# Optimization experiments

Hardware: AMD Instinct MI355X
Metric: run time of the kernel (lower is better)

Reference implementation:

```python
import jax, jax.numpy as jnp
import numpy as np

B, TQ, TKV, D, H = 4, 1024, 2048, 1024, 16
DH = D // H


def setup_inputs() -> dict:
    key = jax.random.key(0)
    ks = jax.random.split(key, 12)
    s = 0.02
    return {
        "x": jax.random.normal(ks[0], (B, TQ, D), jnp.float32),
        "k_cache": jax.random.normal(ks[1], (B, TKV, D), jnp.float32),
        "v_cache": jax.random.normal(ks[2], (B, TKV, D), jnp.float32),
        "mask": jnp.zeros((TQ, TKV), jnp.float32),  # additive attention bias
        "Wq": jax.random.normal(ks[3], (D, D), jnp.float32) * s,
        "bq": jax.random.normal(ks[4], (D,), jnp.float32) * s,
        "Wk": jax.random.normal(ks[5], (D, D), jnp.float32) * s,  # key: no bias (Whisper-style)
        "Wv": jax.random.normal(ks[6], (D, D), jnp.float32) * s,
        "bv": jax.random.normal(ks[7], (D,), jnp.float32) * s,
        "Wo": jax.random.normal(ks[8], (D, D), jnp.float32) * s,
        "bo": jax.random.normal(ks[9], (D,), jnp.float32) * s,
    }


def reference(x, k_cache, v_cache, mask, Wq, bq, Wk, Wv, bv, Wo, bo):
    b, tq, d = x.shape
    scale = (d // H) ** -0.25
    # QKV projections (torch Linear: y = x @ W.T + b)
    q = x @ Wq.T + bq                      # [B,Tq,D]
    k_new = x @ Wk.T                       # [B,Tq,D] (key has no bias)
    v_new = x @ Wv.T + bv                  # [B,Tq,D]
    # KV-cache append: write last Tq positions
    k_cache = k_cache.at[:, -tq:, :].set(k_new)
    v_cache = v_cache.at[:, -tq:, :].set(v_new)
    # split heads
    qh = q.reshape(b, tq, H, DH) * scale           # [B,Tq,H,Dh]
    kh = k_cache.reshape(b, -1, H, DH) * scale     # [B,Tkv,H,Dh]
    vh = v_cache.reshape(b, -1, H, DH)             # [B,Tkv,H,Dh]
    qk = jnp.einsum("bqhd,bkhd->bhqk", qh, kh) + mask  # [B,H,Tq,Tkv]
    w = jax.nn.softmax(qk.astype(jnp.float32), axis=-1).astype(qh.dtype)
    wv = jnp.einsum("bhqk,bkhd->bqhd", w, vh).reshape(b, tq, d)
    out = wv @ Wo.T + bo
    return out, k_cache, v_cache
```

## Files before the change

### kernel.cpp

```cpp
#include <hip/hip_runtime.h>
#include <hip/hip_bf16.h>


typedef __bf16 bf16_t;
typedef __attribute__((ext_vector_type(4))) float f32x4;
typedef __attribute__((ext_vector_type(4))) float f4v;
typedef __attribute__((ext_vector_type(8))) __bf16 bf16x8;
typedef __attribute__((ext_vector_type(4))) __bf16 bf16x4;
typedef __attribute__((ext_vector_type(4))) unsigned short u16x4;

__device__ inline bf16x4 cvt4v(f4v f) {
    bf16x4 o;
    o.x = (bf16_t)f.x; o.y = (bf16_t)f.y; o.z = (bf16_t)f.z; o.w = (bf16_t)f.w;
    return o;
}

__device__ inline void gload_lds16(const void* g, void* s) {
    __builtin_amdgcn_global_load_lds(
        (const __attribute__((address_space(1))) void*)g,
        (__attribute__((address_space(3))) void*)s, 16, 0, 0);
}

__device__ inline bf16x8 ldsr128(const bf16_t* p) {
    bf16x8 d;
    unsigned a = (unsigned)(size_t)(const __attribute__((address_space(3))) bf16_t*)p;
    asm volatile("ds_read_b128 %0, %1" : "=v"(d) : "v"(a));
    return d;
}

#define WAIT_LGKM0 do { asm volatile("s_waitcnt lgkmcnt(0)" ::: "memory"); \
                        __builtin_amdgcn_sched_barrier(0); } while (0)
#define WAIT_VM(n) asm volatile("s_waitcnt vmcnt(" #n ")" ::: "memory")

__device__ inline unsigned cvt_pk_bf16(float lo, float hi) {
    unsigned r;
    asm("v_cvt_pk_bf16_f32 %0, %1, %2" : "=v"(r) : "v"(lo), "v"(hi));
    return r;
}
__device__ inline void pswap32(unsigned& a, unsigned& b) {
    asm("v_permlane32_swap_b32 %0, %1" : "+v"(a), "+v"(b));
}
__device__ inline void pswap16(unsigned& a, unsigned& b) {
    asm("v_permlane16_swap_b32 %0, %1" : "+v"(a), "+v"(b));
}

#if __has_builtin(__builtin_amdgcn_exp2f)
__device__ inline float exp2_fast(float x) { return __builtin_amdgcn_exp2f(x); }
#else
__device__ inline float exp2_fast(float x) { return exp2f(x); }
#endif

__global__ __launch_bounds__(256) void prep_all_k(
        const float* __restrict__ x, const float* __restrict__ kc,
        const float* __restrict__ vc, const float* __restrict__ mask,
        const float* __restrict__ Wq, const float* __restrict__ Wk,
        const float* __restrict__ Wv, const float* __restrict__ Wo,
        const float* __restrict__ bq, const float* __restrict__ bv,
        bf16_t* __restrict__ x_bf, bf16_t* __restrict__ wqkv_bf,
        bf16_t* __restrict__ wo_bf, float* __restrict__ bias,
        bf16_t* __restrict__ maskB, float* __restrict__ kout,
        float* __restrict__ vout, bf16_t* __restrict__ k_bf,
        bf16_t* __restrict__ vT) {
    __shared__ bf16_t tsh[64][65];
    int blk = blockIdx.x, tid = threadIdx.x;
    if (blk < 1024) {
        int kvt = blk >> 6;
        int bh  = blk & 63;
        int b = bh >> 4, h = bh & 15;
        int kv0 = kvt * 64;
        int c = tid & 63, r0 = tid >> 6;
        #pragma unroll
        for (int rr = r0; rr < 64; rr += 4)
            tsh[rr][c] = (bf16_t)vc[((size_t)b * 2048 + kv0 + rr) * 1024 + h * 64 + c];
        __syncthreads();
        #pragma unroll
        for (int dd = r0; dd < 64; dd += 4)
            vT[((size_t)bh * 64 + dd) * 2048 + kv0 + c] = tsh[c][dd];
    } else if (blk < 9216) {
        int i = (blk - 1024) * 256 + tid;
        int which = i >> 20;
        int ii = i & 1048575;
        int b = ii >> 18;
        int r = ii & 262143;
        size_t off = (size_t)b * 2097152 + (size_t)r * 4;
        if (which == 0) {
            f4v f = __builtin_nontemporal_load(reinterpret_cast<const f4v*>(kc + off));
            __builtin_nontemporal_store(f, reinterpret_cast<f4v*>(kout + off));
            __builtin_nontemporal_store(cvt4v(f), reinterpret_cast<bf16x4*>(k_bf + off));
        } else {
            f4v f = *reinterpret_cast<const f4v*>(vc + off);
            __builtin_nontemporal_store(f, reinterpret_cast<f4v*>(vout + off));
        }
    } else if (blk < 13312) {
        int i = (blk - 9216) * 256 + tid;
        f4v f = __builtin_nontemporal_load(reinterpret_cast<const f4v*>(x) + i);
        reinterpret_cast<bf16x4*>(x_bf)[i] = cvt4v(f);
    } else if (blk < 16384) {
        int i = (blk - 13312) * 256 + tid;
        int e0 = i * 4;
        int row = e0 >> 10;
        const float* src;
        if (row < 1024)       src = Wq + e0;
        else if (row < 2048)  src = Wk + (e0 - 1048576);
        else                  src = Wv + (e0 - 2097152);
        f4v f = __builtin_nontemporal_load(reinterpret_cast<const f4v*>(src));
        reinterpret_cast<bf16x4*>(wqkv_bf)[i] = cvt4v(f);
    } else if (blk < 24576) {
        int i = (blk - 16384) * 256 + tid;
        int r   = i & 3;
        int c16 = (i >> 2) & 15;
        int qd  = (i >> 6) & 3;
        int kb  = (i >> 8) & 127;
        int qb  = i >> 15;
        float v = mask[(size_t)(qb * 16 + c16) * 2048 + kb * 16 + qd * 4 + r] * 1.4426950408889634f;
        maskB[i] = (bf16_t)v;
    } else if (blk < 25600) {
        int i = (blk - 24576) * 256 + tid;
        f4v f = __builtin_nontemporal_load(reinterpret_cast<const f4v*>(Wo) + i);
        reinterpret_cast<bf16x4*>(wo_bf)[i] = cvt4v(f);
    } else {
        int i = (blk - 25600) * 256 + tid;
        if (i < 3072) {
            float v;
            if (i < 1024)      v = bq[i];
            else if (i < 2048) v = 0.f;
            else               v = bv[i - 2048];
            bias[i] = v;
        }
    }
}

__global__ __launch_bounds__(256) void transpose_v_k(const float* __restrict__ vout,
                                                     bf16_t* __restrict__ vT) {
    __shared__ bf16_t t[64][65];
    int blk = blockIdx.x;
    int kvt = blk >> 6;
    int bh  = blk & 63;
    int b = bh >> 4, h = bh & 15;
    int kv0 = 1024 + kvt * 64;
    int tid = threadIdx.x;
    int c = tid & 63, r0 = tid >> 6;
    #pragma unroll
    for (int rr = r0; rr < 64; rr += 4)
        t[rr][c] = (bf16_t)vout[((size_t)b * 2048 + kv0 + rr) * 1024 + h * 64 + c];
    __syncthreads();
    #pragma unroll
    for (int dd = r0; dd < 64; dd += 4)
        vT[((size_t)bh * 64 + dd) * 2048 + kv0 + c] = t[c][dd];
}

__global__ __launch_bounds__(512, 2) void gemm8_k(const bf16_t* __restrict__ A,
                                                  const bf16_t* __restrict__ Bw,
                                                  const float* __restrict__ bias,
                                                  bf16_t* __restrict__ q_bf,
                                                  float* __restrict__ kout,
                                                  bf16_t* __restrict__ k_bf,
                                                  float* __restrict__ vout) {
    const int K = 1024;
    __shared__ __align__(16) bf16_t As[2][16384];
    __shared__ __align__(16) bf16_t Bs[2][16384];
    int flat = blockIdx.y * 16 + blockIdx.x;
    int logi = (flat & 7) * 24 + (flat >> 3);
    int m0 = (logi / 12) * 256, n0 = (logi % 12) * 256;
    int tid = threadIdx.x;
    int lane = tid & 63, w = tid >> 6;
    int wrM = w >> 2, wrN = w & 3;
    int col16 = lane & 15, quad = lane >> 4;
    int cx = (quad ^ (col16 & 7)) * 8;

    int sr = tid >> 3;
    int scb = ((tid & 7) ^ (sr & 7)) * 8;
    const bf16_t* ga = A + (size_t)(m0 + sr) * K + scb;
    const bf16_t* gb = Bw + (size_t)(n0 + sr) * K + scb;
    int ldst = sr * 64 + (tid & 7) * 8;

    auto stageA = [&](int d, int kt) {
        size_t ko = (size_t)kt * 64;
        gload_lds16(ga + ko, &As[d][ldst]);
        gload_lds16(ga + 64 * (size_t)K + ko, &As[d][ldst + 4096]);
        gload_lds16(ga + 128 * (size_t)K + ko, &As[d][ldst + 8192]);
        gload_lds16(ga + 192 * (size_t)K + ko, &As[d][ldst + 12288]);
    };
    auto stageB = [&](int d, int kt) {
        size_t ko = (size_t)kt * 64;
        gload_lds16(gb + ko, &Bs[d][ldst]);
        gload_lds16(gb + 64 * (size_t)K + ko, &Bs[d][ldst + 4096]);
        gload_lds16(gb + 128 * (size_t)K + ko, &Bs[d][ldst + 8192]);
        gload_lds16(gb + 192 * (size_t)K + ko, &Bs[d][ldst + 12288]);
    };

    int arow = wrM * 128 + col16;
    int brow = wrN * 64 + col16;

    f32x4 zero = {0.f, 0.f, 0.f, 0.f};
    f32x4 acc[8][4];
    #pragma unroll
    for (int mi = 0; mi < 8; mi++)
        #pragma unroll
        for (int ni = 0; ni < 4; ni++) acc[mi][ni] = zero;

    stageA(0, 0);
    stageB(0, 0);
    stageA(1, 1);
    WAIT_VM(4);
    __builtin_amdgcn_s_barrier();

    for (int kt = 0; kt < 16; kt++) {
        int d = kt & 1;
        const bf16_t* Ad = As[d];
        const bf16_t* Bd = Bs[d];
        bf16x8 a0[4][2], bb0[2][2];
        #pragma unroll
        for (int mi = 0; mi < 4; mi++) {
            const bf16_t* p = &Ad[(arow + mi * 16) * 64];
            a0[mi][0] = ldsr128(p + cx);
            a0[mi][1] = ldsr128(p + (cx ^ 32));
        }
        #pragma unroll
        for (int ni = 0; ni < 2; ni++) {
            const bf16_t* p = &Bd[(brow + ni * 16) * 64];
            bb0[ni][0] = ldsr128(p + cx);
            bb0[ni][1] = ldsr128(p + (cx ^ 32));
        }
        if (kt < 15) stageB(d ^ 1, kt + 1);
        __builtin_amdgcn_s_barrier();
        WAIT_LGKM0;
        __builtin_amdgcn_s_setprio(1);
        #pragma unroll
        for (int mi = 0; mi < 4; mi++)
            #pragma unroll
            for (int ni = 0; ni < 2; ni++) {
                acc[mi][ni] = __builtin_amdgcn_mfma_f32_16x16x32_bf16(a0[mi][0], bb0[ni][0], acc[mi][ni], 0, 0, 0);
                acc[mi][ni] = __builtin_amdgcn_mfma_f32_16x16x32_bf16(a0[mi][1], bb0[ni][1], acc[mi][ni], 0, 0, 0);
            }
        __builtin_amdgcn_s_setprio(0);
        __builtin_amdgcn_s_barrier();
        bf16x8 bb1[2][2];
        #pragma unroll
        for (int ni = 0; ni < 2; ni++) {
            const bf16_t* p = &Bd[(brow + 32 + ni * 16) * 64];
            bb1[ni][0] = ldsr128(p + cx);
            bb1[ni][1] = ldsr128(p + (cx ^ 32));
        }
        __builtin_amdgcn_s_barrier();
        WAIT_LGKM0;
        __builtin_amdgcn_s_setprio(1);
        #pragma unroll
        for (int mi = 0; mi < 4; mi++)
            #pragma unroll
            for (int ni = 0; ni < 2; ni++) {
                acc[mi][ni + 2] = __builtin_amdgcn_mfma_f32_16x16x32_bf16(a0[mi][0], bb1[ni][0], acc[mi][ni + 2], 0, 0, 0);
                acc[mi][ni + 2] = __builtin_amdgcn_mfma_f32_16x16x32_bf16(a0[mi][1], bb1[ni][1], acc[mi][ni + 2], 0, 0, 0);
            }
        __builtin_amdgcn_s_setprio(0);
        __builtin_amdgcn_s_barrier();
        bf16x8 a1[4][2];
        #pragma unroll
        for (int mi = 0; mi < 4; mi++) {
            const bf16_t* p = &Ad[(arow + 64 + mi * 16) * 64];
            a1[mi][0] = ldsr128(p + cx);
            a1[mi][1] = ldsr128(p + (cx ^ 32));
        }
        __builtin_amdgcn_s_barrier();
        WAIT_LGKM0;
        __builtin_amdgcn_s_setprio(1);
        #pragma unroll
        for (int mi = 0; mi < 4; mi++)
            #pragma unroll
            for (int ni = 0; ni < 2; ni++) {
                acc[mi + 4][ni] = __builtin_amdgcn_mfma_f32_16x16x32_bf16(a1[mi][0], bb0[ni][0], acc[mi + 4][ni], 0, 0, 0);
                acc[mi + 4][ni] = __builtin_amdgcn_mfma_f32_16x16x32_bf16(a1[mi][1], bb0[ni][1], acc[mi + 4][ni], 0, 0, 0);
            }
        __builtin_amdgcn_s_setprio(0);
        __builtin_amdgcn_s_barrier();
        if (kt < 14) {
            stageA(d, kt + 2);
            WAIT_VM(4);
        } else {
            WAIT_VM(0);
        }
        __builtin_amdgcn_s_barrier();
        __builtin_amdgcn_s_setprio(1);
        #pragma unroll
        for (int mi = 0; mi < 4; mi++)
            #pragma unroll
            for (int ni = 0; ni < 2; ni++) {
                acc[mi + 4][ni + 2] = __builtin_amdgcn_mfma_f32_16x16x32_bf16(a1[mi][0], bb1[ni][0], acc[mi + 4][ni + 2], 0, 0, 0);
                acc[mi + 4][ni + 2] = __builtin_amdgcn_mfma_f32_16x16x32_bf16(a1[mi][1], bb1[ni][1], acc[mi + 4][ni + 2], 0, 0, 0);
            }
        __builtin_amdgcn_s_setprio(0);
        __builtin_amdgcn_s_barrier();
    }

    int mb = m0 + wrM * 128 + quad * 4;
    int nb = n0 + wrN * 64 + col16;
    if (n0 < 1024) {
        #pragma unroll
        for (int ni = 0; ni < 4; ni++) {
            int gn = nb + ni * 16;
            float bia = bias[gn];
            #pragma unroll
            for (int mi = 0; mi < 8; mi++) {
                int gm = mb + mi * 16;
                #pragma unroll
                for (int r = 0; r < 4; r++)
                    __builtin_nontemporal_store((bf16_t)(acc[mi][ni][r] + bia),
                                                &q_bf[(size_t)(gm + r) * 1024 + gn]);
            }
        }
    } else if (n0 < 2048) {
        #pragma unroll
        for (int ni = 0; ni < 4; ni++) {
            int gn = nb + ni * 16;
            float bia = bias[gn];
            int n2 = gn - 1024;
            #pragma unroll
            for (int mi = 0; mi < 8; mi++) {
                int gm = mb + mi * 16;
                #pragma unroll
                for (int r = 0; r < 4; r++) {
                    int gmr = gm + r;
                    int b = gmr >> 10, t = gmr & 1023;
                    size_t off = ((size_t)b * 2048 + 1024 + t) * 1024 + n2;
                    float v = acc[mi][ni][r] + bia;
                    __builtin_nontemporal_store(v, &kout[off]);
                    __builtin_nontemporal_store((bf16_t)v, &k_bf[off]);
                }
            }
        }
    } else {
        #pragma unroll
        for (int ni = 0; ni < 4; ni++) {
            int gn = nb + ni * 16;
            float bia = bias[gn];
            int n2 = gn - 2048;
            #pragma unroll
            for (int mi = 0; mi < 8; mi++) {
                int gm = mb + mi * 16;
                #pragma unroll
                for (int r = 0; r < 4; r++) {
                    int gmr = gm + r;
                    int b = gmr >> 10, t = gmr & 1023;
                    __builtin_nontemporal_store(acc[mi][ni][r] + bia,
                        &vout[((size_t)b * 2048 + 1024 + t) * 1024 + n2]);
                }
            }
        }
    }
}

__global__ __launch_bounds__(256) void gemm_wo_k(const bf16_t* __restrict__ A,
                                                 const bf16_t* __restrict__ Bw,
                                                 const float* __restrict__ bias,
                                                 float* __restrict__ out0) {
    const int K = 1024;
    __shared__ __align__(16) bf16_t As[2][4096];
    __shared__ __align__(16) bf16_t Bs[2][4096];
    int m0 = blockIdx.x * 128, n0 = blockIdx.y * 128;
    int tid = threadIdx.x;
    int lane = tid & 63, w = tid >> 6;
    int wr = w >> 1, wc = w & 1;
    int col16 = lane & 15, quad = lane >> 4;

    int srow = tid >> 2;
    int scol = ((tid & 3) ^ ((srow >> 1) & 3)) * 8;
    const bf16_t* ga = A + (size_t)(m0 + srow) * K + scol;
    const bf16_t* gb = Bw + (size_t)(n0 + srow) * K + scol;

    int qsw = (quad ^ ((col16 >> 1) & 3)) * 8;

    f32x4 zero = {0.f, 0.f, 0.f, 0.f};
    f32x4 acc[4][4];
    #pragma unroll
    for (int mi = 0; mi < 4; mi++)
        #pragma unroll
        for (int ni = 0; ni < 4; ni++) acc[mi][ni] = zero;

    auto stageg = [&](int d, int k) {
        gload_lds16(ga + k, &As[d][tid * 8]);
        gload_lds16(ga + (size_t)64 * K + k, &As[d][tid * 8 + 2048]);
        gload_lds16(gb + k, &Bs[d][tid * 8]);
        gload_lds16(gb + (size_t)64 * K + k, &Bs[d][tid * 8 + 2048]);
    };

    stageg(0, 0);
    __syncthreads();
    for (int kb = 0; kb < 32; kb++) {
        int cur = kb & 1;
        if (kb < 31) stageg(cur ^ 1, (kb + 1) * 32);
        bf16x8 af[4], bfr[4];
        #pragma unroll
        for (int mi = 0; mi < 4; mi++)
            af[mi] = ldsr128(&As[cur][(wr * 64 + mi * 16 + col16) * 32 + qsw]);
        #pragma unroll
        for (int ni = 0; ni < 4; ni++)
            bfr[ni] = ldsr128(&Bs[cur][(wc * 64 + ni * 16 + col16) * 32 + qsw]);
        WAIT_LGKM0;
        #pragma unroll
        for (int mi = 0; mi < 4; mi++)
            #pragma unroll
            for (int ni = 0; ni < 4; ni++)
                acc[mi][ni] = __builtin_amdgcn_mfma_f32_16x16x32_bf16(
                    af[mi], bfr[ni], acc[mi][ni], 0, 0, 0);
        __syncthreads();
    }

    int mbase = m0 + wr * 64 + quad * 4;
    int nbase = n0 + wc * 64 + col16;
    #pragma unroll
    for (int ni = 0; ni < 4; ni++) {
        int gn = nbase + ni * 16;
        float bia = bias[gn];
        #pragma unroll
        for (int mi = 0; mi < 4; mi++) {
            int gm = mbase + mi * 16;
            #pragma unroll
            for (int r = 0; r < 4; r++)
                __builtin_nontemporal_store(acc[mi][ni][r] + bia,
                                            &out0[(size_t)(gm + r) * 1024 + gn]);
        }
    }
}

__global__ __launch_bounds__(512, 4) void attn_k(const bf16_t* __restrict__ qbf,
                                                 const bf16_t* __restrict__ kbf,
                                                 const bf16_t* __restrict__ vT,
                                                 const bf16_t* __restrict__ maskB,
                                                 bf16_t* __restrict__ wv) {
    __shared__ __align__(16) bf16_t Ks[2][4096];
    __shared__ __align__(16) bf16_t Vs[2][4096];
    int logical = (blockIdx.x & 7) * 64 + (blockIdx.x >> 3);
    int bh = logical >> 3;
    int qtb = logical & 7;
    int b = bh >> 4, h = bh & 15;
    int tid = threadIdx.x, w = tid >> 6, lane = tid & 63;
    int col16 = lane & 15, quad = lane >> 4;
    int c7 = col16 & 7;
    int cx = (quad ^ c7) * 8;
    int qr0 = qtb * 128 + w * 16;

    int sr = tid >> 3, sc = (tid & 7) ^ ((tid >> 3) & 7);
    const bf16_t* kg = kbf + ((size_t)b * 2048 + sr) * 1024 + h * 64 + sc * 8;
    const bf16_t* vg = vT + ((size_t)bh * 64 + sr) * 2048 + sc * 8;
    auto stage = [&](int d, int kv0) {
        gload_lds16(kg + (size_t)kv0 * 1024, &Ks[d][tid * 8]);
        gload_lds16(vg + kv0, &Vs[d][tid * 8]);
    };

    const bf16_t* qrow = qbf + ((size_t)b * 1024 + qr0 + col16) * 1024 + h * 64;
    bf16x8 aq0 = *reinterpret_cast<const bf16x8*>(qrow + quad * 8);
    bf16x8 aq1 = *reinterpret_cast<const bf16x8*>(qrow + 32 + quad * 8);

    const bf16_t* mbase = maskB + (size_t)(qtb * 8 + w) * 32768 + quad * 64 + col16 * 4;

    f32x4 zero = {0.f, 0.f, 0.f, 0.f};
    f32x4 oacc[4];
    #pragma unroll
    for (int dt = 0; dt < 4; dt++) oacc[dt] = zero;
    float lrow = 0.f;

    stage(0, 0);
    __syncthreads();

    for (int t = 0; t < 32; t++) {
        int cur = t & 1;
        if (t < 31) stage(cur ^ 1, (t + 1) * 64);
        bf16x8 kf[4][2];
        #pragma unroll
        for (int nt = 0; nt < 4; nt++) {
            const bf16_t* kr = &Ks[cur][(nt * 16 + col16) * 64];
            kf[nt][0] = ldsr128(kr + cx);
            kf[nt][1] = ldsr128(kr + (cx ^ 32));
        }
        u16x4 m4[4];
        #pragma unroll
        for (int nt = 0; nt < 4; nt++)
            m4[nt] = *reinterpret_cast<const u16x4*>(mbase + (size_t)(t * 4 + nt) * 256);
        WAIT_LGKM0;
        f32x4 sv[4];
        __builtin_amdgcn_s_setprio(1);
        #pragma unroll
        for (int nt = 0; nt < 4; nt++) {
            sv[nt] = __builtin_amdgcn_mfma_f32_16x16x32_bf16(kf[nt][0], aq0, zero, 0, 0, 0);
            sv[nt] = __builtin_amdgcn_mfma_f32_16x16x32_bf16(kf[nt][1], aq1, sv[nt], 0, 0, 0);
        }
        __builtin_amdgcn_s_setprio(0);
        unsigned pk[4][2];
        #pragma unroll
        for (int nt = 0; nt < 4; nt++) {
            float p[4];
            #pragma unroll
            for (int r = 0; r < 4; r++) {
                float mv = __builtin_bit_cast(float, (unsigned)m4[nt][r] << 16);
                p[r] = exp2_fast(fmaf(sv[nt][r], 0.18033688011112042f, mv));
                lrow += p[r];
            }
            pk[nt][0] = cvt_pk_bf16(p[0], p[1]);
            pk[nt][1] = cvt_pk_bf16(p[2], p[3]);
        }
        union PB { unsigned u[4]; bf16x8 v; };
        PB pf0, pf1;
        {
            unsigned a0 = pk[0][0], b0 = pk[1][0];
            pswap32(a0, b0); pswap16(a0, b0);
            pf0.u[0] = a0; pf0.u[2] = b0;
            unsigned a1 = pk[0][1], b1 = pk[1][1];
            pswap32(a1, b1); pswap16(a1, b1);
            pf0.u[1] = a1; pf0.u[3] = b1;
            unsigned a2 = pk[2][0], b2 = pk[3][0];
            pswap32(a2, b2); pswap16(a2, b2);
            pf1.u[0] = a2; pf1.u[2] = b2;
            unsigned a3 = pk[2][1], b3 = pk[3][1];
            pswap32(a3, b3); pswap16(a3, b3);
            pf1.u[1] = a3; pf1.u[3] = b3;
        }
        bf16x8 vf[4][2];
        #pragma unroll
        for (int dt = 0; dt < 4; dt++) {
            const bf16_t* vr = &Vs[cur][(dt * 16 + col16) * 64];
            vf[dt][0] = ldsr128(vr + cx);
            vf[dt][1] = ldsr128(vr + (cx ^ 32));
        }
        WAIT_LGKM0;
        __builtin_amdgcn_s_setprio(1);
        #pragma unroll
        for (int dt = 0; dt < 4; dt++) {
            oacc[dt] = __builtin_amdgcn_mfma_f32_16x16x32_bf16(vf[dt][0], pf0.v, oacc[dt], 0, 0, 0);
            oacc[dt] = __builtin_amdgcn_mfma_f32_16x16x32_bf16(vf[dt][1], pf1.v, oacc[dt], 0, 0, 0);
        }
        __builtin_amdgcn_s_setprio(0);
        __syncthreads();
    }

    lrow += __shfl_xor(lrow, 16);
    lrow += __shfl_xor(lrow, 32);
    float inv = 1.f / lrow;
    bf16_t* orow = wv + ((size_t)b * 1024 + qr0 + col16) * 1024 + h * 64 + quad * 4;
    #pragma unroll
    for (int dt = 0; dt < 4; dt++) {
        bf16x4 o4;
        #pragma unroll
        for (int r = 0; r < 4; r++) o4[r] = (bf16_t)(oacc[dt][r] * inv);
        *reinterpret_cast<bf16x4*>(orow + dt * 16) = o4;
    }
}


extern "C" void kernel_launch(void* const* d_in, const int* in_sizes, int n_in,
                              void* d_out, int out_size, void* d_ws, size_t ws_size,
                              hipStream_t stream) {
    const float* x    = (const float*)d_in[0];
    const float* kc   = (const float*)d_in[1];
    const float* vc   = (const float*)d_in[2];
    const float* mask = (const float*)d_in[3];
    const float* Wq   = (const float*)d_in[4];
    const float* bq   = (const float*)d_in[5];
    const float* Wk   = (const float*)d_in[6];
    const float* Wv   = (const float*)d_in[7];
    const float* bv   = (const float*)d_in[8];
    const float* Wo   = (const float*)d_in[9];
    const float* bo   = (const float*)d_in[10];

    float* out0 = (float*)d_out;
    float* kout = out0 + 4194304;
    float* vout = out0 + 12582912;

    char* ws = (char*)d_ws;
    bf16_t* x_bf     = (bf16_t*)(ws);
    bf16_t* wqkv_bf  = (bf16_t*)(ws + 8388608);
    bf16_t* wo_bf    = (bf16_t*)(ws + 14680064);
    float*  bias_qkv = (float*)(ws + 16777216);
    bf16_t* q_bf     = (bf16_t*)(ws + 16789504);
    bf16_t* k_bf     = (bf16_t*)(ws + 25178112);
    bf16_t* vT_bf    = (bf16_t*)(ws + 41955328);
    bf16_t* wv_bf    = (bf16_t*)(ws + 58732544);
    bf16_t* maskB    = (bf16_t*)(ws + 67108864);

    prep_all_k<<<25612, 256, 0, stream>>>(x, kc, vc, mask, Wq, Wk, Wv, Wo, bq, bv,
                                          x_bf, wqkv_bf, wo_bf, bias_qkv, maskB,
                                          kout, vout, k_bf, vT_bf);
    gemm8_k<<<dim3(16, 12), 512, 0, stream>>>(x_bf, wqkv_bf, bias_qkv,
                                              q_bf, kout, k_bf, vout);
    transpose_v_k<<<1024, 256, 0, stream>>>(vout, vT_bf);
    attn_k<<<512, 512, 0, stream>>>(q_bf, k_bf, vT_bf, maskB, wv_bf);
    gemm_wo_k<<<dim3(32, 8), 256, 0, stream>>>(wv_bf, wo_bf, bo, out0);
}
```

Before: 317.0 us.

## Transpose MFMA operands for vectorized epilogue stores and fuse v-cache copy into transpose

The MFMA operand order in both GEMM kernels is swapped so each lane holds four consecutive output columns instead of four rows. The epilogues can then write 16-byte f32x4 and 8-byte bf16x4 vectors, loading the bias as a vector, instead of scattered scalar stores. Separately, the v-cache copy to vout is folded into the transpose block that already reads vc, which removes a second full read of v_cache and shrinks the prep grid. The fused copy now uses scalar per-element stores rather than 16-byte vector stores, which may cost some store efficiency.

```diff
diff --git a/kernel.cpp b/kernel.cpp
--- a/kernel.cpp
+++ b/kernel.cpp
@@ -70,33 +70,30 @@
         int kv0 = kvt * 64;
         int c = tid & 63, r0 = tid >> 6;
         #pragma unroll
-        for (int rr = r0; rr < 64; rr += 4)
-            tsh[rr][c] = (bf16_t)vc[((size_t)b * 2048 + kv0 + rr) * 1024 + h * 64 + c];
+        for (int rr = r0; rr < 64; rr += 4) {
+            size_t gi = ((size_t)b * 2048 + kv0 + rr) * 1024 + h * 64 + c;
+            float fv = vc[gi];
+            tsh[rr][c] = (bf16_t)fv;
+            __builtin_nontemporal_store(fv, &vout[gi]);
+        }
         __syncthreads();
         #pragma unroll
         for (int dd = r0; dd < 64; dd += 4)
             vT[((size_t)bh * 64 + dd) * 2048 + kv0 + c] = tsh[c][dd];
+    } else if (blk < 5120) {
+        int i = (blk - 1024) * 256 + tid;
+        int b = i >> 18;
+        int r = i & 262143;
+        size_t off = (size_t)b * 2097152 + (size_t)r * 4;
+        f4v f = __builtin_nontemporal_load(reinterpret_cast<const f4v*>(kc + off));
+        __builtin_nontemporal_store(f, reinterpret_cast<f4v*>(kout + off));
+        __builtin_nontemporal_store(cvt4v(f), reinterpret_cast<bf16x4*>(k_bf + off));
     } else if (blk < 9216) {
-        int i = (blk - 1024) * 256 + tid;
-        int which = i >> 20;
-        int ii = i & 1048575;
-        int b = ii >> 18;
-        int r = ii & 262143;
-        size_t off = (size_t)b * 2097152 + (size_t)r * 4;
-        if (which == 0) {
-            f4v f = __builtin_nontemporal_load(reinterpret_cast<const f4v*>(kc + off));
-            __builtin_nontemporal_store(f, reinterpret_cast<f4v*>(kout + off));
-            __builtin_nontemporal_store(cvt4v(f), reinterpret_cast<bf16x4*>(k_bf + off));
-        } else {
-            f4v f = *reinterpret_cast<const f4v*>(vc + off);
-            __builtin_nontemporal_store(f, reinterpret_cast<f4v*>(vout + off));
-        }
-    } else if (blk < 13312) {
-        int i = (blk - 9216) * 256 + tid;
+        int i = (blk - 5120) * 256 + tid;
         f4v f = __builtin_nontemporal_load(reinterpret_cast<const f4v*>(x) + i);
         reinterpret_cast<bf16x4*>(x_bf)[i] = cvt4v(f);
-    } else if (blk < 16384) {
-        int i = (blk - 13312) * 256 + tid;
+    } else if (blk < 12288) {
+        int i = (blk - 9216) * 256 + tid;
         int e0 = i * 4;
         int row = e0 >> 10;
         const float* src;
@@ -105,8 +102,8 @@
         else                  src = Wv + (e0 - 2097152);
         f4v f = __builtin_nontemporal_load(reinterpret_cast<const f4v*>(src));
         reinterpret_cast<bf16x4*>(wqkv_bf)[i] = cvt4v(f);
-    } else if (blk < 24576) {
-        int i = (blk - 16384) * 256 + tid;
+    } else if (blk < 20480) {
+        int i = (blk - 12288) * 256 + tid;
         int r   = i & 3;
         int c16 = (i >> 2) & 15;
         int qd  = (i >> 6) & 3;
@@ -114,12 +111,12 @@
         int qb  = i >> 15;
         float v = mask[(size_t)(qb * 16 + c16) * 2048 + kb * 16 + qd * 4 + r] * 1.4426950408889634f;
         maskB[i] = (bf16_t)v;
-    } else if (blk < 25600) {
-        int i = (blk - 24576) * 256 + tid;
+    } else if (blk < 21504) {
+        int i = (blk - 20480) * 256 + tid;
         f4v f = __builtin_nontemporal_load(reinterpret_cast<const f4v*>(Wo) + i);
         reinterpret_cast<bf16x4*>(wo_bf)[i] = cvt4v(f);
     } else {
-        int i = (blk - 25600) * 256 + tid;
+        int i = (blk - 21504) * 256 + tid;
         if (i < 3072) {
             float v;
             if (i < 1024)      v = bq[i];
@@ -230,8 +227,8 @@
         for (int mi = 0; mi < 4; mi++)
             #pragma unroll
             for (int ni = 0; ni < 2; ni++) {
-                acc[mi][ni] = __builtin_amdgcn_mfma_f32_16x16x32_bf16(a0[mi][0], bb0[ni][0], acc[mi][ni], 0, 0, 0);
-                acc[mi][ni] = __builtin_amdgcn_mfma_f32_16x16x32_bf16(a0[mi][1], bb0[ni][1], acc[mi][ni], 0, 0, 0);
+                acc[mi][ni] = __builtin_amdgcn_mfma_f32_16x16x32_bf16(bb0[ni][0], a0[mi][0], acc[mi][ni], 0, 0, 0);
+                acc[mi][ni] = __builtin_amdgcn_mfma_f32_16x16x32_bf16(bb0[ni][1], a0[mi][1], acc[mi][ni], 0, 0, 0);
             }
         __builtin_amdgcn_s_setprio(0);
         __builtin_amdgcn_s_barrier();
@@ -249,8 +246,8 @@
         for (int mi = 0; mi < 4; mi++)
             #pragma unroll
             for (int ni = 0; ni < 2; ni++) {
-                acc[mi][ni + 2] = __builtin_amdgcn_mfma_f32_16x16x32_bf16(a0[mi][0], bb1[ni][0], acc[mi][ni + 2], 0, 0, 0);
-                acc[mi][ni + 2] = __builtin_amdgcn_mfma_f32_16x16x32_bf16(a0[mi][1], bb1[ni][1], acc[mi][ni + 2], 0, 0, 0);
+                acc[mi][ni + 2] = __builtin_amdgcn_mfma_f32_16x16x32_bf16(bb1[ni][0], a0[mi][0], acc[mi][ni + 2], 0, 0, 0);
+                acc[mi][ni + 2] = __builtin_amdgcn_mfma_f32_16x16x32_bf16(bb1[ni][1], a0[mi][1], acc[mi][ni + 2], 0, 0, 0);
             }
         __builtin_amdgcn_s_setprio(0);
         __builtin_amdgcn_s_barrier();
@@ -268,8 +265,8 @@
         for (int mi = 0; mi < 4; mi++)
             #pragma unroll
             for (int ni = 0; ni < 2; ni++) {
-                acc[mi + 4][ni] = __builtin_amdgcn_mfma_f32_16x16x32_bf16(a1[mi][0], bb0[ni][0], acc[mi + 4][ni], 0, 0, 0);
-                acc[mi + 4][ni] = __builtin_amdgcn_mfma_f32_16x16x32_bf16(a1[mi][1], bb0[ni][1], acc[mi + 4][ni], 0, 0, 0);
+                acc[mi + 4][ni] = __builtin_amdgcn_mfma_f32_16x16x32_bf16(bb0[ni][0], a1[mi][0], acc[mi + 4][ni], 0, 0, 0);
+                acc[mi + 4][ni] = __builtin_amdgcn_mfma_f32_16x16x32_bf16(bb0[ni][1], a1[mi][1], acc[mi + 4][ni], 0, 0, 0);
             }
         __builtin_amdgcn_s_setprio(0);
         __builtin_amdgcn_s_barrier();
@@ -285,65 +282,61 @@
         for (int mi = 0; mi < 4; mi++)
             #pragma unroll
             for (int ni = 0; ni < 2; ni++) {
-                acc[mi + 4][ni + 2] = __builtin_amdgcn_mfma_f32_16x16x32_bf16(a1[mi][0], bb1[ni][0], acc[mi + 4][ni + 2], 0, 0, 0);
-                acc[mi + 4][ni + 2] = __builtin_amdgcn_mfma_f32_16x16x32_bf16(a1[mi][1], bb1[ni][1], acc[mi + 4][ni + 2], 0, 0, 0);
+                acc[mi + 4][ni + 2] = __builtin_amdgcn_mfma_f32_16x16x32_bf16(bb1[ni][0], a1[mi][0], acc[mi + 4][ni + 2], 0, 0, 0);
+                acc[mi + 4][ni + 2] = __builtin_amdgcn_mfma_f32_16x16x32_bf16(bb1[ni][1], a1[mi][1], acc[mi + 4][ni + 2], 0, 0, 0);
             }
         __builtin_amdgcn_s_setprio(0);
         __builtin_amdgcn_s_barrier();
     }
 
-    int mb = m0 + wrM * 128 + quad * 4;
-    int nb = n0 + wrN * 64 + col16;
+    int mbW = m0 + wrM * 128;
+    int nbW = n0 + wrN * 64;
     if (n0 < 1024) {
         #pragma unroll
         for (int ni = 0; ni < 4; ni++) {
-            int gn = nb + ni * 16;
-            float bia = bias[gn];
+            int gn = nbW + ni * 16 + quad * 4;
+            f32x4 b4 = *reinterpret_cast<const f32x4*>(bias + gn);
             #pragma unroll
             for (int mi = 0; mi < 8; mi++) {
-                int gm = mb + mi * 16;
+                int gm = mbW + mi * 16 + col16;
+                bf16x4 o;
                 #pragma unroll
-                for (int r = 0; r < 4; r++)
-                    __builtin_nontemporal_store((bf16_t)(acc[mi][ni][r] + bia),
-                                                &q_bf[(size_t)(gm + r) * 1024 + gn]);
+                for (int r = 0; r < 4; r++) o[r] = (bf16_t)(acc[mi][ni][r] + b4[r]);
+                __builtin_nontemporal_store(o,
+                    reinterpret_cast<bf16x4*>(&q_bf[(size_t)gm * 1024 + gn]));
             }
         }
     } else if (n0 < 2048) {
         #pragma unroll
         for (int ni = 0; ni < 4; ni++) {
-            int gn = nb + ni * 16;
-            float bia = bias[gn];
+            int gn = nbW + ni * 16 + quad * 4;
+            f32x4 b4 = *reinterpret_cast<const f32x4*>(bias + gn);
             int n2 = gn - 1024;
             #pragma unroll
             for (int mi = 0; mi < 8; mi++) {
-                int gm = mb + mi * 16;
+                int gm = mbW + mi * 16 + col16;
+                int b = gm >> 10, t = gm & 1023;
+                size_t off = ((size_t)b * 2048 + 1024 + t) * 1024 + n2;
+                f32x4 v = acc[mi][ni] + b4;
+                bf16x4 o;
                 #pragma unroll
-                for (int r = 0; r < 4; r++) {
-                    int gmr = gm + r;
-                    int b = gmr >> 10, t = gmr & 1023;
-                    size_t off = ((size_t)b * 2048 + 1024 + t) * 1024 + n2;
-                    float v = acc[mi][ni][r] + bia;
-                    __builtin_nontemporal_store(v, &kout[off]);
-                    __builtin_nontemporal_store((bf16_t)v, &k_bf[off]);
-                }
+                for (int r = 0; r < 4; r++) o[r] = (bf16_t)v[r];
+                __builtin_nontemporal_store(v, reinterpret_cast<f32x4*>(&kout[off]));
+                __builtin_nontemporal_store(o, reinterpret_cast<bf16x4*>(&k_bf[off]));
             }
         }
     } else {
         #pragma unroll
         for (int ni = 0; ni < 4; ni++) {
-            int gn = nb + ni * 16;
-            float bia = bias[gn];
+            int gn = nbW + ni * 16 + quad * 4;
+            f32x4 b4 = *reinterpret_cast<const f32x4*>(bias + gn);
             int n2 = gn - 2048;
             #pragma unroll
             for (int mi = 0; mi < 8; mi++) {
-                int gm = mb + mi * 16;
-                #pragma unroll
-                for (int r = 0; r < 4; r++) {
-                    int gmr = gm + r;
-                    int b = gmr >> 10, t = gmr & 1023;
-                    __builtin_nontemporal_store(acc[mi][ni][r] + bia,
-                        &vout[((size_t)b * 2048 + 1024 + t) * 1024 + n2]);
-                }
+                int gm = mbW + mi * 16 + col16;
+                int b = gm >> 10, t = gm & 1023;
+                f32x4 v = acc[mi][ni] + b4;
+                *reinterpret_cast<f32x4*>(&vout[((size_t)b * 2048 + 1024 + t) * 1024 + n2]) = v;
             }
         }
     }
@@ -401,23 +394,19 @@
             #pragma unroll
             for (int ni = 0; ni < 4; ni++)
                 acc[mi][ni] = __builtin_amdgcn_mfma_f32_16x16x32_bf16(
-                    af[mi], bfr[ni], acc[mi][ni], 0, 0, 0);
+                    bfr[ni], af[mi], acc[mi][ni], 0, 0, 0);
         __syncthreads();
     }
 
-    int mbase = m0 + wr * 64 + quad * 4;
-    int nbase = n0 + wc * 64 + col16;
     #pragma unroll
     for (int ni = 0; ni < 4; ni++) {
-        int gn = nbase + ni * 16;
-        float bia = bias[gn];
+        int gn = n0 + wc * 64 + ni * 16 + quad * 4;
+        f32x4 b4 = *reinterpret_cast<const f32x4*>(bias + gn);
         #pragma unroll
         for (int mi = 0; mi < 4; mi++) {
-            int gm = mbase + mi * 16;
-            #pragma unroll
-            for (int r = 0; r < 4; r++)
-                __builtin_nontemporal_store(acc[mi][ni][r] + bia,
-                                            &out0[(size_t)(gm + r) * 1024 + gn]);
+            int gm = m0 + wr * 64 + mi * 16 + col16;
+            f32x4 o = acc[mi][ni] + b4;
+            __builtin_nontemporal_store(o, reinterpret_cast<f32x4*>(&out0[(size_t)gm * 1024 + gn]));
         }
     }
 }
@@ -576,7 +565,7 @@
     bf16_t* wv_bf    = (bf16_t*)(ws + 58732544);
     bf16_t* maskB    = (bf16_t*)(ws + 67108864);
 
-    prep_all_k<<<25612, 256, 0, stream>>>(x, kc, vc, mask, Wq, Wk, Wv, Wo, bq, bv,
+    prep_all_k<<<21516, 256, 0, stream>>>(x, kc, vc, mask, Wq, Wk, Wv, Wo, bq, bv,
                                           x_bf, wqkv_bf, wo_bf, bias_qkv, maskB,
                                           kout, vout, k_bf, vT_bf);
     gemm8_k<<<dim3(16, 12), 512, 0, stream>>>(x_bf, wqkv_bf, bias_qkv,
```

Measured after the change: 312.5 us. No clear change (-1.4%).
